# Kernel tuning notes

Hardware: AMD Instinct MI355X
Metric: run time of the kernel (lower is better)

The kernel has to match this reference:

```python
import jax, jax.numpy as jnp
import numpy as np

B, N, D, P, H = 16, 1024, 512, 512, 8
E = P // H  # head dim = 64


def layer_norm(x, g, b, eps=1e-5):
    mu = jnp.mean(x, axis=-1, keepdims=True)
    var = jnp.var(x, axis=-1, keepdims=True)
    return (x - mu) * jax.lax.rsqrt(var + eps) * g + b


def setup_inputs() -> dict:
    key = jax.random.key(0)
    ks = jax.random.split(key, 12)
    s = 0.02
    inp = {
        "x": jax.random.normal(ks[0], (B, N, D), dtype=jnp.float32),
        "Wq": jax.random.normal(ks[1], (D, P), dtype=jnp.float32) * s,
        "bq": jnp.zeros((P,), jnp.float32),
        "Wk": jax.random.normal(ks[2], (D, P), dtype=jnp.float32) * s,
        "bk": jnp.zeros((P,), jnp.float32),
        "Wv": jax.random.normal(ks[3], (D, P), dtype=jnp.float32) * s,
        "bv": jnp.zeros((P,), jnp.float32),
        "Wo": jax.random.normal(ks[4], (P, D), dtype=jnp.float32) * s,
        "bo": jnp.zeros((D,), jnp.float32),
        "ln1_g": jnp.ones((D,), jnp.float32),
        "ln1_b": jnp.zeros((D,), jnp.float32),
        "W1": jax.random.normal(ks[5], (D, 4 * D), dtype=jnp.float32) * s,
        "b1": jnp.zeros((4 * D,), jnp.float32),
        "W2": jax.random.normal(ks[6], (4 * D, D), dtype=jnp.float32) * s,
        "b2": jnp.zeros((D,), jnp.float32),
        "ln2_g": jnp.ones((D,), jnp.float32),
        "ln2_b": jnp.zeros((D,), jnp.float32),
    }
    return inp


def reference(x, Wq, bq, Wk, bk, Wv, bv, Wo, bo, ln1_g, ln1_b, W1, b1, W2, b2, ln2_g, ln2_b):
    # dropout layers are identity in eval mode
    q = (x @ Wq + bq).reshape(B, N, H, E)
    k = (x @ Wk + bk).reshape(B, N, H, E)
    v = (x @ Wv + bv).reshape(B, N, H, E)
    scale = 1.0 / jnp.sqrt(jnp.float32(E))
    scores = jnp.einsum('blhe,bshe->bhls', q, k)  # [B,H,L,S]
    A = jax.nn.softmax(scale * scores, axis=-1)
    V = jnp.einsum('bhls,bshd->blhd', A, v).reshape(B, N, P)
    att = V @ Wo + bo
    x1 = layer_norm(x + att, ln1_g, ln1_b)
    # FFN: 1x1 convs over channel dim == per-token linears, exact GELU
    ff = jax.nn.gelu(x1 @ W1 + b1, approximate=False) @ W2 + b2
    return layer_norm(x1 + ff, ln2_g, ln2_b)
```

## Files before the change

kernel.cpp:

```cpp
#include <hip/hip_runtime.h>
#include <hip/hip_bf16.h>

typedef __hip_bfloat16 bf16;
typedef __bf16 bf16x8 __attribute__((ext_vector_type(8)));
typedef __bf16 bf16x4 __attribute__((ext_vector_type(4)));
typedef float f32x4 __attribute__((ext_vector_type(4)));

static __device__ __forceinline__ f32x4 mfma16(bf16x8 a, bf16x8 b, f32x4 c) {
  return __builtin_amdgcn_mfma_f32_16x16x32_bf16(a, b, c, 0, 0, 0);
}
static __device__ __forceinline__ bf16x8 ld8(const bf16* p) {
  return *reinterpret_cast<const bf16x8*>(p);
}
static __device__ __forceinline__ float toF(float v) { return v; }
static __device__ __forceinline__ float toF(bf16 v) { return __bfloat162float(v); }
static __device__ __forceinline__ void stF(float* p, float v) { *p = v; }
static __device__ __forceinline__ void stF(bf16* p, float v) { *p = __float2bfloat16(v); }

typedef __attribute__((address_space(1))) void gvoid;
typedef __attribute__((address_space(3))) void lvoid;
static __device__ __forceinline__ void gl2lds16(const bf16* g, bf16* l) {
  __builtin_amdgcn_global_load_lds((gvoid*)g, (lvoid*)l, 16, 0, 0);
}

__global__ __launch_bounds__(256) void cvt_kernel(const float* __restrict__ in,
                                                  bf16* __restrict__ out) {
  long i = (long)blockIdx.x * 256 + threadIdx.x;
  float4 v = reinterpret_cast<const float4*>(in)[i];
  bf16x4 o;
  o[0] = __float2bfloat16(v.x); o[1] = __float2bfloat16(v.y);
  o[2] = __float2bfloat16(v.z); o[3] = __float2bfloat16(v.w);
  reinterpret_cast<bf16x4*>(out)[i] = o;
}

__global__ void prep_weights(const float* __restrict__ Wq, const float* __restrict__ Wk,
                             const float* __restrict__ Wv, const float* __restrict__ Wo,
                             const float* __restrict__ W1, const float* __restrict__ W2,
                             bf16* __restrict__ Wtqkv, bf16* __restrict__ WtO,
                             bf16* __restrict__ Wt1, bf16* __restrict__ Wt2) {
  int id = blockIdx.x;
  const float* in;
  bf16* out;
  int K, N, n0, k0;
  if (id < 1024) {
    int which = id >> 8, t = id & 255;
    K = 512; N = 512;
    n0 = (t & 15) * 32; k0 = (t >> 4) * 32;
    if (which == 0)      { in = Wq; out = Wtqkv; }
    else if (which == 1) { in = Wk; out = Wtqkv + (size_t)512 * 512; }
    else if (which == 2) { in = Wv; out = Wtqkv + (size_t)1024 * 512; }
    else                 { in = Wo; out = WtO; }
  } else if (id < 2048) {
    int t = id - 1024;
    in = W1; out = Wt1; K = 512; N = 2048;
    n0 = (t & 63) * 32; k0 = (t >> 6) * 32;
  } else {
    int t = id - 2048;
    in = W2; out = Wt2; K = 2048; N = 512;
    n0 = (t & 15) * 32; k0 = (t >> 4) * 32;
  }
  __shared__ float tile[32][33];
  int tx = threadIdx.x, ty = threadIdx.y;
#pragma unroll
  for (int j = 0; j < 32; j += 8)
    tile[ty + j][tx] = in[(long)(k0 + ty + j) * N + n0 + tx];
  __syncthreads();
#pragma unroll
  for (int j = 0; j < 32; j += 8)
    out[(long)(n0 + ty + j) * K + k0 + tx] = __float2bfloat16(tile[tx][ty + j]);
}

template <int MODE>
__global__ __launch_bounds__(256) void gemm_kernel(
    const bf16* __restrict__ A, const bf16* __restrict__ Wt,
    const float* __restrict__ b0, const float* __restrict__ b1_,
    const float* __restrict__ b2_, bf16* C0, bf16* C1, bf16* C2,
    int K, int ldc, int mmask, int mshift) {
  __shared__ alignas(16) bf16 As[3][128 * 32];
  __shared__ alignas(16) bf16 Bs[3][128 * 32];
  const int tid = threadIdx.x;
  const int wave = tid >> 6, lane = tid & 63;
  const int lr = lane & 15, lq = lane >> 4;
  const int L = blockIdx.x;
  const int m0 = (L & mmask) * 128, n0 = (L >> mshift) * 128;
  const int wm = (wave >> 1) * 64, wn = (wave & 1) * 64;

  const int srow0 = (wave * 2) * 16 + (lane >> 2);
  const int srow1 = (wave * 2 + 1) * 16 + (lane >> 2);
  const int scol = (lane & 3) * 8;
  const bf16* Ag0 = A + (long)(m0 + srow0) * K + scol;
  const bf16* Ag1 = A + (long)(m0 + srow1) * K + scol;
  const bf16* Bg0 = Wt + (long)(n0 + srow0) * K + scol;
  const bf16* Bg1 = Wt + (long)(n0 + srow1) * K + scol;
  const int so0 = (wave * 2) * 16 * 32;
  const int so1 = (wave * 2 + 1) * 16 * 32;

  f32x4 acc[4][4] = {};

  auto stage = [&](int k0, int buf) {
    gl2lds16(Ag0 + k0, &As[buf][so0]);
    gl2lds16(Ag1 + k0, &As[buf][so1]);
    gl2lds16(Bg0 + k0, &Bs[buf][so0]);
    gl2lds16(Bg1 + k0, &Bs[buf][so1]);
  };

  stage(0, 0);
  stage(32, 1);

  const int nk = K >> 5;
  int cur = 0, sb = 2;
  for (int t = 0; t < nk; ++t) {
    if (t < nk - 1) {
      asm volatile("s_waitcnt vmcnt(4)" ::: "memory");
    } else {
      asm volatile("s_waitcnt vmcnt(0)" ::: "memory");
    }
    __builtin_amdgcn_s_barrier();
    if (t < nk - 2) stage((t + 2) << 5, sb);

    bf16x8 af[4], bfr[4];
#pragma unroll
    for (int i = 0; i < 4; ++i) af[i] = ld8(&As[cur][(wm + i * 16 + lr) * 32 + lq * 8]);
#pragma unroll
    for (int j = 0; j < 4; ++j) bfr[j] = ld8(&Bs[cur][(wn + j * 16 + lr) * 32 + lq * 8]);
#pragma unroll
    for (int i = 0; i < 4; ++i)
#pragma unroll
      for (int j = 0; j < 4; ++j) acc[i][j] = mfma16(af[i], bfr[j], acc[i][j]);

    cur = (cur == 2) ? 0 : cur + 1;
    sb = (sb == 2) ? 0 : sb + 1;
  }

  const float* bias = b0;
  bf16* C = C0;
  int cb = n0;
  bool vmode = false;
  if (MODE == 2) {
    if (n0 >= 1024)     { bias = b2_; C = C2; cb = n0 - 1024; vmode = true; }
    else if (n0 >= 512) { bias = b1_; C = C1; cb = n0 - 512; }
  }

#pragma unroll
  for (int i = 0; i < 4; ++i) {
#pragma unroll
    for (int j = 0; j < 4; ++j) {
      int col = cb + wn + j * 16 + lr;
      float bv = bias[col];
#pragma unroll
      for (int rr = 0; rr < 4; ++rr) {
        int row = m0 + wm + i * 16 + lq * 4 + rr;
        float v = acc[i][j][rr] + bv;
        if (MODE == 1) v = 0.5f * v * (1.0f + erff(v * 0.70710678118654752f));
        if (MODE == 2 && vmode) {
          int hh = col >> 6, e = col & 63;
          int bb = row >> 10, tok = row & 1023;
          C[(((long)((bb * 8 + hh) * 64 + e)) << 10) + tok] = __float2bfloat16(v);
        } else {
          C[(long)row * ldc + col] = __float2bfloat16(v);
        }
      }
    }
  }
}

__global__ __launch_bounds__(256) void attn_splitk(
    const bf16* __restrict__ Q, const bf16* __restrict__ Km,
    const bf16* __restrict__ Vt, bf16* __restrict__ Op,
    float* __restrict__ lsum) {
  constexpr int SP = 72;
  __shared__ alignas(16) bf16 Pall[4][64 * SP];
  __shared__ alignas(16) bf16 Ks[2][2][64][32];
  __shared__ alignas(16) bf16 Vs[2][2][64][32];
  const int tid = threadIdx.x;
  const int wave = tid >> 6, lane = tid & 63;
  const int lr = lane & 15, lq = lane >> 4;
  const int L = blockIdx.x;
  const int bh = ((L >> 6) << 3) | (L & 7);
  const int qh = (L >> 3) & 7;
  const int qc = qh & 3, half = qh >> 2;
  const int h = bh & 7, b = bh >> 3;
  const int q0 = qc * 256 + wave * 64;
  bf16* P = Pall[wave];
  const float Cc = 0.18033688011112042f;

  bf16x8 qf[4][2];
#pragma unroll
  for (int qs = 0; qs < 4; ++qs) {
    const bf16* qrow = Q + (long)(b * 1024 + q0 + qs * 16 + lr) * 512 + h * 64;
    qf[qs][0] = ld8(qrow + lq * 8);
    qf[qs][1] = ld8(qrow + 32 + lq * 8);
  }
  const bf16* kbase = Km + (long)(b * 1024 + half * 512) * 512 + h * 64;
  const bf16* vbase = Vt + (long)((b * 8 + h) * 64) * 1024 + half * 512;

  const int sr = wave * 16 + (lane >> 2);
  const int sc = (lane & 3) * 8;
  const bf16* Kg = kbase + (long)sr * 512 + sc;
  const bf16* Vg = vbase + (long)sr * 1024 + sc;

  auto stage = [&](int kb, int p) {
#pragma unroll
    for (int kk = 0; kk < 2; ++kk)
      gl2lds16(Kg + (long)kb * 64 * 512 + kk * 32, &Ks[p][kk][wave * 16][0]);
#pragma unroll
    for (int kk = 0; kk < 2; ++kk)
      gl2lds16(Vg + kb * 64 + kk * 32, &Vs[p][kk][wave * 16][0]);
  };

  bf16x8 ones;
#pragma unroll
  for (int k = 0; k < 8; ++k) ones[k] = __float2bfloat16(1.0f);

  f32x4 oacc[4][4] = {};
  f32x4 lacc[4] = {};

  stage(0, 0);
  __syncthreads();

  int p = 0;
  for (int kb = 0; kb < 8; ++kb) {
    if (kb < 7) stage(kb + 1, p ^ 1);
#pragma unroll
    for (int kt = 0; kt < 4; ++kt) {
      bf16x8 kf0 = ld8(&Ks[p][0][kt * 16 + lr][lq * 8]);
      bf16x8 kf1 = ld8(&Ks[p][1][kt * 16 + lr][lq * 8]);
#pragma unroll
      for (int qs = 0; qs < 4; ++qs) {
        f32x4 t = {};
        t = mfma16(kf0, qf[qs][0], t);
        t = mfma16(kf1, qf[qs][1], t);
        bf16x4 pk;
#pragma unroll
        for (int rr = 0; rr < 4; ++rr) pk[rr] = __float2bfloat16(exp2f(t[rr] * Cc));
        *reinterpret_cast<bf16x4*>(&P[(qs * 16 + lr) * SP + kt * 16 + lq * 4]) = pk;
      }
    }
    __builtin_amdgcn_sched_barrier(0);
    bf16x8 pf[4][2];
#pragma unroll
    for (int qs = 0; qs < 4; ++qs) {
      pf[qs][0] = ld8(&P[(qs * 16 + lr) * SP + lq * 8]);
      pf[qs][1] = ld8(&P[(qs * 16 + lr) * SP + 32 + lq * 8]);
    }
#pragma unroll
    for (int qs = 0; qs < 4; ++qs) {
      lacc[qs] = mfma16(pf[qs][0], ones, lacc[qs]);
      lacc[qs] = mfma16(pf[qs][1], ones, lacc[qs]);
    }
#pragma unroll
    for (int j0 = 0; j0 < 4; ++j0) {
      bf16x8 vf0 = ld8(&Vs[p][0][j0 * 16 + lr][lq * 8]);
      bf16x8 vf1 = ld8(&Vs[p][1][j0 * 16 + lr][lq * 8]);
#pragma unroll
      for (int qs = 0; qs < 4; ++qs) {
        oacc[qs][j0] = mfma16(pf[qs][0], vf0, oacc[qs][j0]);
        oacc[qs][j0] = mfma16(pf[qs][1], vf1, oacc[qs][j0]);
      }
    }
    __builtin_amdgcn_sched_barrier(0);
    __syncthreads();
    p ^= 1;
  }

  bf16* Oh = Op + (size_t)half * ((size_t)16384 * 512);
#pragma unroll
  for (int qs = 0; qs < 4; ++qs)
#pragma unroll
    for (int rr = 0; rr < 4; ++rr)
#pragma unroll
      for (int j0 = 0; j0 < 4; ++j0)
        Oh[(long)(b * 1024 + q0 + qs * 16 + lq * 4 + rr) * 512 + h * 64 + j0 * 16 + lr] =
            __float2bfloat16(oacc[qs][j0][rr]);
  if (lr == 0) {
    float* lp = lsum + (size_t)half * 131072 + ((size_t)(b * 8 + h) << 10);
#pragma unroll
    for (int qs = 0; qs < 4; ++qs)
#pragma unroll
      for (int rr = 0; rr < 4; ++rr)
        lp[q0 + qs * 16 + lq * 4 + rr] = lacc[qs][rr];
  }
}

__global__ __launch_bounds__(256) void attn_combine(
    const bf16* __restrict__ Op, const float* __restrict__ lsum,
    bf16* __restrict__ O) {
  long i = (long)blockIdx.x * 256 + threadIdx.x;
  long idx = i * 8;
  int tok = (int)(idx >> 9), col = (int)(idx & 511);
  int b = tok >> 10, q = tok & 1023, h = col >> 6;
  int li = (b * 8 + h) * 1024 + q;
  float inv = 1.0f / (lsum[li] + lsum[131072 + li]);
  bf16x8 a = ld8(Op + idx);
  bf16x8 c = ld8(Op + (size_t)16384 * 512 + idx);
  bf16x8 o;
#pragma unroll
  for (int k = 0; k < 8; ++k)
    o[k] = __float2bfloat16(((float)a[k] + (float)c[k]) * inv);
  *reinterpret_cast<bf16x8*>(O + idx) = o;
}

__global__ __launch_bounds__(256) void attn_kernel(
    const bf16* Q, const bf16* __restrict__ Km,
    const bf16* __restrict__ Vt, bf16* O) {
  constexpr int SP = 72;
  __shared__ alignas(16) bf16 Pall[4][64 * SP];
  const int tid = threadIdx.x;
  const int wave = tid >> 6, lane = tid & 63;
  const int lr = lane & 15, lq = lane >> 4;
  const int L = blockIdx.x;
  const int bh = ((L >> 5) << 3) | (L & 7);
  const int qc = (L >> 3) & 3;
  const int h = bh & 7, b = bh >> 3;
  const int q0 = qc * 256 + wave * 64;
  bf16* P = Pall[wave];
  const float Cc = 0.18033688011112042f;

  bf16x8 qf[4][2];
#pragma unroll
  for (int qs = 0; qs < 4; ++qs) {
    const bf16* qrow = Q + (long)(b * 1024 + q0 + qs * 16 + lr) * 512 + h * 64;
    qf[qs][0] = ld8(qrow + lq * 8);
    qf[qs][1] = ld8(qrow + 32 + lq * 8);
  }
  const bf16* kbase = Km + (long)(b * 1024) * 512 + h * 64;
  const bf16* vbase = Vt + (long)((b * 8 + h) * 64) * 1024;

  bf16x8 ones;
#pragma unroll
  for (int k = 0; k < 8; ++k) ones[k] = __float2bfloat16(1.0f);

  f32x4 oacc[4][4] = {};
  f32x4 lacc[4] = {};

  for (int kb = 0; kb < 16; ++kb) {
#pragma unroll
    for (int kt = 0; kt < 4; ++kt) {
      const bf16* krow = kbase + (long)(kb * 64 + kt * 16 + lr) * 512;
      bf16x8 kf0 = ld8(krow + lq * 8);
      bf16x8 kf1 = ld8(krow + 32 + lq * 8);
#pragma unroll
      for (int qs = 0; qs < 4; ++qs) {
        f32x4 t = {};
        t = mfma16(kf0, qf[qs][0], t);
        t = mfma16(kf1, qf[qs][1], t);
        bf16x4 pk;
#pragma unroll
        for (int rr = 0; rr < 4; ++rr) pk[rr] = __float2bfloat16(exp2f(t[rr] * Cc));
        *reinterpret_cast<bf16x4*>(&P[(qs * 16 + lr) * SP + kt * 16 + lq * 4]) = pk;
      }
    }
    __builtin_amdgcn_sched_barrier(0);
    bf16x8 pf[4][2];
#pragma unroll
    for (int qs = 0; qs < 4; ++qs) {
      pf[qs][0] = ld8(&P[(qs * 16 + lr) * SP + lq * 8]);
      pf[qs][1] = ld8(&P[(qs * 16 + lr) * SP + 32 + lq * 8]);
    }
#pragma unroll
    for (int qs = 0; qs < 4; ++qs) {
      lacc[qs] = mfma16(pf[qs][0], ones, lacc[qs]);
      lacc[qs] = mfma16(pf[qs][1], ones, lacc[qs]);
    }
#pragma unroll
    for (int j0 = 0; j0 < 4; ++j0) {
      const bf16* vrow = vbase + (long)(j0 * 16 + lr) * 1024 + kb * 64;
      bf16x8 vf0 = ld8(vrow + lq * 8);
      bf16x8 vf1 = ld8(vrow + 32 + lq * 8);
#pragma unroll
      for (int qs = 0; qs < 4; ++qs) {
        oacc[qs][j0] = mfma16(pf[qs][0], vf0, oacc[qs][j0]);
        oacc[qs][j0] = mfma16(pf[qs][1], vf1, oacc[qs][j0]);
      }
    }
    __builtin_amdgcn_sched_barrier(0);
  }

#pragma unroll
  for (int qs = 0; qs < 4; ++qs)
#pragma unroll
    for (int rr = 0; rr < 4; ++rr) {
      float lv = 1.0f / lacc[qs][rr];
#pragma unroll
      for (int j0 = 0; j0 < 4; ++j0)
        O[(long)(b * 1024 + q0 + qs * 16 + lq * 4 + rr) * 512 + h * 64 + j0 * 16 + lr] =
            __float2bfloat16(oacc[qs][j0][rr] * lv);
    }
}

template <typename TX, typename TO>
__global__ __launch_bounds__(256) void add_ln_kernel(
    const TX* __restrict__ X, const bf16* __restrict__ Y,
    const float* __restrict__ g, const float* __restrict__ bb,
    TO* __restrict__ out) {
  const int row = blockIdx.x, t = threadIdx.x;
  __shared__ float s1[4], s2[4];
  long base = (long)row * 512;
  float v0 = toF(X[base + t]) + toF(Y[base + t]);
  float v1 = toF(X[base + 256 + t]) + toF(Y[base + 256 + t]);
  float s = v0 + v1, q = v0 * v0 + v1 * v1;
#pragma unroll
  for (int o = 32; o > 0; o >>= 1) {
    s += __shfl_down(s, o);
    q += __shfl_down(q, o);
  }
  int wv = t >> 6;
  if ((t & 63) == 0) { s1[wv] = s; s2[wv] = q; }
  __syncthreads();
  float St = s1[0] + s1[1] + s1[2] + s1[3];
  float Qt = s2[0] + s2[1] + s2[2] + s2[3];
  float mean = St * (1.f / 512.f);
  float var = Qt * (1.f / 512.f) - mean * mean;
  float rs = rsqrtf(var + 1e-5f);
  stF(&out[base + t], (v0 - mean) * rs * g[t] + bb[t]);
  stF(&out[base + 256 + t], (v1 - mean) * rs * g[256 + t] + bb[256 + t]);
}

extern "C" void kernel_launch(void* const* d_in, const int* in_sizes, int n_in,
                              void* d_out, int out_size, void* d_ws, size_t ws_size,
                              hipStream_t stream) {
  const float* x    = (const float*)d_in[0];
  const float* Wq   = (const float*)d_in[1];
  const float* bq   = (const float*)d_in[2];
  const float* Wk   = (const float*)d_in[3];
  const float* bk   = (const float*)d_in[4];
  const float* Wv   = (const float*)d_in[5];
  const float* bv   = (const float*)d_in[6];
  const float* Wo   = (const float*)d_in[7];
  const float* bo   = (const float*)d_in[8];
  const float* ln1g = (const float*)d_in[9];
  const float* ln1b = (const float*)d_in[10];
  const float* W1   = (const float*)d_in[11];
  const float* b1   = (const float*)d_in[12];
  const float* W2   = (const float*)d_in[13];
  const float* b2   = (const float*)d_in[14];
  const float* ln2g = (const float*)d_in[15];
  const float* ln2b = (const float*)d_in[16];
  float* out = (float*)d_out;

  char* ws = (char*)d_ws;
  size_t off = 0;
  auto alloc = [&](size_t bytes) {
    char* p = ws + off;
    off += (bytes + 255) & ~(size_t)255;
    return (bf16*)p;
  };
  bf16* Wtqkv = alloc((size_t)1536 * 512 * 2);
  bf16* WtO   = alloc((size_t)512 * 512 * 2);
  bf16* Wt1   = alloc((size_t)512 * 2048 * 2);
  bf16* Wt2   = alloc((size_t)2048 * 512 * 2);
  const size_t SB = (size_t)16384 * 512 * 2;

  dim3 tb(32, 8);

  if (ws_size >= (size_t)104 * 1024 * 1024) {
    bf16* xb  = alloc(SB);
    bf16* kb  = alloc(SB);
    bf16* qb  = alloc(SB);
    bf16* vtb = alloc(SB);
    bf16* p0  = alloc(SB);
    bf16* p1  = alloc(SB);
    float* lsum = (float*)alloc((size_t)2 * 131072 * 4);
    bf16* ff1 = qb;
    bf16* ff2 = xb;
    (void)p1;

    cvt_kernel<<<8192, 256, 0, stream>>>(x, xb);
    prep_weights<<<3072, tb, 0, stream>>>(Wq, Wk, Wv, Wo, W1, W2,
                                          Wtqkv, WtO, Wt1, Wt2);
    gemm_kernel<2><<<1536, 256, 0, stream>>>(xb, Wtqkv, bq, bk, bv,
                                             qb, kb, vtb, 512, 512, 127, 7);
    attn_splitk<<<1024, 256, 0, stream>>>(qb, kb, vtb, p0, lsum);
    attn_combine<<<4096, 256, 0, stream>>>(p0, lsum, qb);
    gemm_kernel<0><<<512, 256, 0, stream>>>(qb, WtO, bo, nullptr, nullptr,
                                            vtb, nullptr, nullptr, 512, 512, 127, 7);
    add_ln_kernel<bf16, bf16><<<16384, 256, 0, stream>>>(xb, vtb, ln1g, ln1b, kb);
    gemm_kernel<1><<<2048, 256, 0, stream>>>(kb, Wt1, b1, nullptr, nullptr,
                                             ff1, nullptr, nullptr, 512, 2048, 127, 7);
    gemm_kernel<0><<<512, 256, 0, stream>>>(ff1, Wt2, b2, nullptr, nullptr,
                                            ff2, nullptr, nullptr, 2048, 512, 127, 7);
    add_ln_kernel<bf16, float><<<16384, 256, 0, stream>>>(kb, ff2, ln2g, ln2b, out);
  } else {
    bf16* xb  = alloc(SB);
    bf16* kb  = alloc(SB);
    bf16* qb  = alloc(SB);
    bf16* vtb = alloc(SB);
    bf16* fb  = alloc(SB / 2);
    bf16* ff1 = qb;

    cvt_kernel<<<8192, 256, 0, stream>>>(x, xb);
    prep_weights<<<3072, tb, 0, stream>>>(Wq, Wk, Wv, Wo, W1, W2,
                                          Wtqkv, WtO, Wt1, Wt2);
    gemm_kernel<2><<<1536, 256, 0, stream>>>(xb, Wtqkv, bq, bk, bv,
                                             qb, kb, vtb, 512, 512, 127, 7);
    attn_kernel<<<512, 256, 0, stream>>>(qb, kb, vtb, qb);
    gemm_kernel<0><<<512, 256, 0, stream>>>(qb, WtO, bo, nullptr, nullptr,
                                            vtb, nullptr, nullptr, 512, 512, 127, 7);
    add_ln_kernel<bf16, bf16><<<16384, 256, 0, stream>>>(xb, vtb, ln1g, ln1b, kb);

    for (int hh = 0; hh < 2; ++hh) {
      const bf16* x1h = kb + (size_t)hh * 8192 * 512;
      gemm_kernel<1><<<1024, 256, 0, stream>>>(x1h, Wt1, b1, nullptr, nullptr,
                                               ff1, nullptr, nullptr, 512, 2048, 63, 6);
      gemm_kernel<0><<<256, 256, 0, stream>>>(ff1, Wt2, b2, nullptr, nullptr,
                                              fb, nullptr, nullptr, 2048, 512, 63, 6);
      add_ln_kernel<bf16, float><<<8192, 256, 0, stream>>>(x1h, fb, ln2g, ln2b,
                                                           out + (size_t)hh * 8192 * 512);
    }
  }
}
```

Baseline: 386.8 us.

## Replace erff GELU with polynomial approximation and halve attention P tile

The exact erff in the FFN GELU epilogue is replaced with an Abramowitz-Stegun polynomial erf approximation using one reciprocal and one fast exp. Separately, the attention kernel processes each 64-key block in two 32-key halves, so the per-wave P scratch in LDS shrinks (row pitch 72 to 40) and fewer P fragments are live in registers. This cuts transcendental cost and LDS/register footprint, with a small accuracy risk in GELU (max error around 1e-7 on erf) and extra sched barriers between halves.

New measurement: 401.6 us. 3.8% more time.

```diff
diff --git a/kernel.cpp b/kernel.cpp
--- a/kernel.cpp
+++ b/kernel.cpp
@@ -16,6 +16,16 @@
 static __device__ __forceinline__ float toF(bf16 v) { return __bfloat162float(v); }
 static __device__ __forceinline__ void stF(float* p, float v) { *p = v; }
 static __device__ __forceinline__ void stF(bf16* p, float v) { *p = __float2bfloat16(v); }
+
+static __device__ __forceinline__ float fast_gelu(float x) {
+  float y = fabsf(x) * 0.70710678118654752f;
+  float t = 1.0f / fmaf(0.3275911f, y, 1.0f);
+  float p = t * fmaf(t, fmaf(t, fmaf(t, fmaf(t, 1.061405429f, -1.453152027f),
+                                     1.421413741f), -0.284496736f), 0.254829592f);
+  float e = __expf(-y * y);
+  float erfv = copysignf(1.0f - p * e, x);
+  return 0.5f * x * (1.0f + erfv);
+}
 
 typedef __attribute__((address_space(1))) void gvoid;
 typedef __attribute__((address_space(3))) void lvoid;
@@ -151,7 +161,7 @@
       for (int rr = 0; rr < 4; ++rr) {
         int row = m0 + wm + i * 16 + lq * 4 + rr;
         float v = acc[i][j][rr] + bv;
-        if (MODE == 1) v = 0.5f * v * (1.0f + erff(v * 0.70710678118654752f));
+        if (MODE == 1) v = fast_gelu(v);
         if (MODE == 2 && vmode) {
           int hh = col >> 6, e = col & 63;
           int bb = row >> 10, tok = row & 1023;
@@ -168,7 +178,7 @@
     const bf16* __restrict__ Q, const bf16* __restrict__ Km,
     const bf16* __restrict__ Vt, bf16* __restrict__ Op,
     float* __restrict__ lsum) {
-  constexpr int SP = 72;
+  constexpr int SP = 40;
   __shared__ alignas(16) bf16 Pall[4][64 * SP];
   __shared__ alignas(16) bf16 Ks[2][2][64][32];
   __shared__ alignas(16) bf16 Vs[2][2][64][32];
@@ -222,43 +232,37 @@
   for (int kb = 0; kb < 8; ++kb) {
     if (kb < 7) stage(kb + 1, p ^ 1);
 #pragma unroll
-    for (int kt = 0; kt < 4; ++kt) {
-      bf16x8 kf0 = ld8(&Ks[p][0][kt * 16 + lr][lq * 8]);
-      bf16x8 kf1 = ld8(&Ks[p][1][kt * 16 + lr][lq * 8]);
-#pragma unroll
-      for (int qs = 0; qs < 4; ++qs) {
-        f32x4 t = {};
-        t = mfma16(kf0, qf[qs][0], t);
-        t = mfma16(kf1, qf[qs][1], t);
-        bf16x4 pk;
-#pragma unroll
-        for (int rr = 0; rr < 4; ++rr) pk[rr] = __float2bfloat16(exp2f(t[rr] * Cc));
-        *reinterpret_cast<bf16x4*>(&P[(qs * 16 + lr) * SP + kt * 16 + lq * 4]) = pk;
+    for (int hf = 0; hf < 2; ++hf) {
+#pragma unroll
+      for (int kt = 0; kt < 2; ++kt) {
+        bf16x8 kf0 = ld8(&Ks[p][0][hf * 32 + kt * 16 + lr][lq * 8]);
+        bf16x8 kf1 = ld8(&Ks[p][1][hf * 32 + kt * 16 + lr][lq * 8]);
+#pragma unroll
+        for (int qs = 0; qs < 4; ++qs) {
+          f32x4 t = {};
+          t = mfma16(kf0, qf[qs][0], t);
+          t = mfma16(kf1, qf[qs][1], t);
+          bf16x4 pk;
+#pragma unroll
+          for (int rr = 0; rr < 4; ++rr) pk[rr] = __float2bfloat16(exp2f(t[rr] * Cc));
+          *reinterpret_cast<bf16x4*>(&P[(qs * 16 + lr) * SP + kt * 16 + lq * 4]) = pk;
+        }
       }
-    }
-    __builtin_amdgcn_sched_barrier(0);
-    bf16x8 pf[4][2];
-#pragma unroll
-    for (int qs = 0; qs < 4; ++qs) {
-      pf[qs][0] = ld8(&P[(qs * 16 + lr) * SP + lq * 8]);
-      pf[qs][1] = ld8(&P[(qs * 16 + lr) * SP + 32 + lq * 8]);
-    }
-#pragma unroll
-    for (int qs = 0; qs < 4; ++qs) {
-      lacc[qs] = mfma16(pf[qs][0], ones, lacc[qs]);
-      lacc[qs] = mfma16(pf[qs][1], ones, lacc[qs]);
-    }
-#pragma unroll
-    for (int j0 = 0; j0 < 4; ++j0) {
-      bf16x8 vf0 = ld8(&Vs[p][0][j0 * 16 + lr][lq * 8]);
-      bf16x8 vf1 = ld8(&Vs[p][1][j0 * 16 + lr][lq * 8]);
-#pragma unroll
-      for (int qs = 0; qs < 4; ++qs) {
-        oacc[qs][j0] = mfma16(pf[qs][0], vf0, oacc[qs][j0]);
-        oacc[qs][j0] = mfma16(pf[qs][1], vf1, oacc[qs][j0]);
+      __builtin_amdgcn_sched_barrier(0);
+      bf16x8 pf[4];
+#pragma unroll
+      for (int qs = 0; qs < 4; ++qs) pf[qs] = ld8(&P[(qs * 16 + lr) * SP + lq * 8]);
+#pragma unroll
+      for (int qs = 0; qs < 4; ++qs) lacc[qs] = mfma16(pf[qs], ones, lacc[qs]);
+#pragma unroll
+      for (int j0 = 0; j0 < 4; ++j0) {
+        bf16x8 vf = ld8(&Vs[p][hf][j0 * 16 + lr][lq * 8]);
+#pragma unroll
+        for (int qs = 0; qs < 4; ++qs)
+          oacc[qs][j0] = mfma16(pf[qs], vf, oacc[qs][j0]);
       }
-    }
-    __builtin_amdgcn_sched_barrier(0);
+      __builtin_amdgcn_sched_barrier(0);
+    }
     __syncthreads();
     p ^= 1;
   }
```
